# Optimization experiments

Hardware: AMD Instinct MI355X
Metric: run time of the kernel (lower is better)

## Reference

```python
import jax, jax.numpy as jnp
import numpy as np

D_MODEL = 1024
N_HEADS = 16
EPS = 1e-6


def setup_inputs() -> dict:
    key = jax.random.key(0)
    k1, k2, k3 = jax.random.split(key, 3)
    B, T, D = 2, 2048, D_MODEL
    x = jax.random.normal(k1, (B, T, D), dtype=jnp.float32)
    # learned params
    norm_weight = jnp.ones((D,), dtype=jnp.float32)
    qkv_w = jax.random.normal(k2, (3 * D, D), dtype=jnp.float32) * (1.0 / np.sqrt(D))
    out_w = jax.random.normal(k3, (D, D), dtype=jnp.float32) * (1.0 / np.sqrt(D))
    return {"x": x, "norm_weight": norm_weight, "qkv_w": qkv_w, "out_w": out_w}


def reference(x, norm_weight, qkv_w, out_w):
    B, T, D = x.shape
    H = N_HEADS
    d = D // H
    # RMSNorm
    ms = jnp.mean(x * x, axis=-1, keepdims=True)
    xn = x * jax.lax.rsqrt(ms + EPS) * norm_weight
    # QKV projection (Linear, no bias): y = x @ W^T
    qkv = jnp.einsum('btd,ed->bte', xn, qkv_w)  # (B,T,3D)
    q, k, v = jnp.split(qkv, 3, axis=-1)
    q = q.reshape(B, T, H, d)
    k = k.reshape(B, T, H, d)
    v = v.reshape(B, T, H, d)
    # scores (B,H,T,T) with causal mask
    scores = jnp.einsum('bqhd,bkhd->bhqk', q, k) / np.sqrt(d).astype(np.float32)
    causal = jnp.tril(jnp.ones((T, T), dtype=bool))
    scores = jnp.where(causal[None, None], scores, -jnp.inf)
    probs = jax.nn.softmax(scores, axis=-1)
    ctx = jnp.einsum('bhqk,bkhd->bqhd', probs, v)  # (B,T,H,d)
    out = ctx.reshape(B, T, D)
    out = jnp.einsum('btd,ed->bte', out, out_w)
    return out
```

## Files before the change

kernel.cpp:

```cpp
#include <hip/hip_runtime.h>
#include <stdint.h>

#define B_SZ 2
#define T_SZ 2048
#define DMODEL 1024
#define HCNT 16
#define HD 64
#define MROWS (B_SZ * T_SZ)

typedef __attribute__((ext_vector_type(8))) __bf16 bf16x8;
typedef __attribute__((ext_vector_type(4))) __bf16 bf16x4;
typedef __attribute__((ext_vector_type(4))) float f32x4;
typedef __attribute__((ext_vector_type(8))) unsigned short u16x8;

__device__ __forceinline__ unsigned short f2bf(float f) {
  union { float f; uint32_t u; } v; v.f = f;
  uint32_t u = v.u;
  u += 0x7fffu + ((u >> 16) & 1u);
  return (unsigned short)(u >> 16);
}

__device__ __forceinline__ float fexp2(float x) {
#if __has_builtin(__builtin_amdgcn_exp2f)
  return __builtin_amdgcn_exp2f(x);
#else
  return exp2f(x);
#endif
}

__device__ __forceinline__ void gld_lds16(const void* g, void* l) {
  __builtin_amdgcn_global_load_lds((__attribute__((address_space(1))) void*)(uintptr_t)g,
                                   (__attribute__((address_space(3))) void*)l, 16, 0, 0);
}

__global__ __launch_bounds__(256)
void cvt_all(const float* __restrict__ qkv_w, const float* __restrict__ out_w,
             unsigned short* __restrict__ dst) {
  int i = blockIdx.x * 256 + threadIdx.x;
  const int n1 = 3 * DMODEL * DMODEL / 4;
  float4 v = (i < n1) ? ((const float4*)qkv_w)[i] : ((const float4*)out_w)[i - n1];
  ushort4 o;
  o.x = f2bf(v.x); o.y = f2bf(v.y); o.z = f2bf(v.z); o.w = f2bf(v.w);
  ((ushort4*)dst)[i] = o;
}

__global__ __launch_bounds__(256)
void rmsnorm_bf16(const float* __restrict__ x, const float* __restrict__ w,
                  unsigned short* __restrict__ xn) {
  const int row = blockIdx.x;
  const int t = threadIdx.x;
  float4 v = ((const float4*)(x + (size_t)row * DMODEL))[t];
  float ss = v.x * v.x + v.y * v.y + v.z * v.z + v.w * v.w;
#pragma unroll
  for (int o = 1; o < 64; o <<= 1) ss += __shfl_xor(ss, o, 64);
  __shared__ float red[4];
  if ((t & 63) == 0) red[t >> 6] = ss;
  __syncthreads();
  float tot = red[0] + red[1] + red[2] + red[3];
  float scale = rsqrtf(tot * (1.0f / (float)DMODEL) + 1e-6f);
  float4 wv = ((const float4*)w)[t];
  ushort4 o;
  o.x = f2bf(v.x * scale * wv.x);
  o.y = f2bf(v.y * scale * wv.y);
  o.z = f2bf(v.z * scale * wv.z);
  o.w = f2bf(v.w * scale * wv.w);
  ((ushort4*)(xn + (size_t)row * DMODEL))[t] = o;
}

__device__ __forceinline__ void stage128x64(const unsigned short* g, int ldg,
                                            unsigned short* lds, int tid) {
  const int wave = tid >> 6;
#pragma unroll
  for (int i = 0; i < 4; ++i) {
    int row = i * 32 + (tid >> 3);
    const unsigned short* gp = g + (size_t)row * ldg + (((tid & 7) ^ (row & 7)) << 3);
    gld_lds16(gp, lds + i * 2048 + wave * 512);
  }
}

template <int F32OUT>
__global__ __launch_bounds__(256, 2)
void gemm_bt(const unsigned short* __restrict__ A, const unsigned short* __restrict__ B,
             void* __restrict__ Cv, int M, int N, int K, int nbx) {
  __shared__ __align__(16) unsigned short As[2][128 * 64];
  __shared__ __align__(16) unsigned short Bs[2][128 * 64];
  const int t = threadIdx.x, wave = t >> 6, lane = t & 63;
  const int cpx = gridDim.x >> 3;
  const int swz = (blockIdx.x & 7) * cpx + (blockIdx.x >> 3);
  const int m0 = (swz / nbx) * 128, n0 = (swz % nbx) * 128;
  const int wr = wave >> 1, wc = wave & 1;
  const int c = lane & 15, qg = lane >> 4;
  f32x4 acc[4][4] = {};
  const int nk = K >> 6;
  stage128x64(A + (size_t)m0 * K, K, As[0], t);
  stage128x64(B + (size_t)n0 * K, K, Bs[0], t);
  __syncthreads();
  int buf = 0;
  for (int kt = 0; kt < nk; ++kt) {
    if (kt + 1 < nk) {
      stage128x64(A + (size_t)m0 * K + (kt + 1) * 64, K, As[buf ^ 1], t);
      stage128x64(B + (size_t)n0 * K + (kt + 1) * 64, K, Bs[buf ^ 1], t);
    }
#pragma unroll
    for (int kk = 0; kk < 2; ++kk) {
      bf16x8 af[4], bfr[4];
#pragma unroll
      for (int mi = 0; mi < 4; ++mi) {
        int row = wr * 64 + mi * 16 + c;
        af[mi] = *(const bf16x8*)&As[buf][row * 64 + (((kk * 4 + qg) ^ (row & 7)) << 3)];
      }
#pragma unroll
      for (int ni = 0; ni < 4; ++ni) {
        int row = wc * 64 + ni * 16 + c;
        bfr[ni] = *(const bf16x8*)&Bs[buf][row * 64 + (((kk * 4 + qg) ^ (row & 7)) << 3)];
      }
#pragma unroll
      for (int mi = 0; mi < 4; ++mi)
#pragma unroll
        for (int ni = 0; ni < 4; ++ni)
          acc[mi][ni] = __builtin_amdgcn_mfma_f32_16x16x32_bf16(af[mi], bfr[ni], acc[mi][ni], 0, 0, 0);
    }
    __syncthreads();
    buf ^= 1;
  }
  const int cr = qg * 4;
#pragma unroll
  for (int mi = 0; mi < 4; ++mi)
#pragma unroll
    for (int ni = 0; ni < 4; ++ni) {
      int row = m0 + wr * 64 + mi * 16 + cr;
      int col = n0 + wc * 64 + ni * 16 + c;
      if (F32OUT) {
        float* C = (float*)Cv;
#pragma unroll
        for (int r = 0; r < 4; ++r) C[(size_t)(row + r) * N + col] = acc[mi][ni][r];
      } else {
        unsigned short* C = (unsigned short*)Cv;
#pragma unroll
        for (int r = 0; r < 4; ++r) C[(size_t)(row + r) * N + col] = f2bf(acc[mi][ni][r]);
      }
    }
}

__global__ __launch_bounds__(512, 2)
void attn_causal(const unsigned short* __restrict__ qkv, unsigned short* __restrict__ ctx) {
  __shared__ __align__(16) unsigned short Ks[2][128 * 64];
  __shared__ __align__(16) unsigned short Vt[2][2][64 * 72];
  __shared__ __align__(16) unsigned short Pl[8][32 * 136];
  const int tid = threadIdx.x, wave = tid >> 6, lane = tid & 63;
  const int id = blockIdx.x;
  const int bh = (id & 7) | ((id >> 6) << 3);
  const int p = (id >> 3) & 7;
  const int b = bh >> 4, h = bh & 15;
  const int q0a = p * 128 + wave * 16;
  const int q0b = (15 - p) * 128 + wave * 16;
  const int nit = 16 - p;
  const int c = lane & 15, qg = lane >> 4;
  const size_t base = (size_t)b * T_SZ * 3 * DMODEL;
  const int koffK = DMODEL + h * HD;
  const int koffV = 2 * DMODEL + h * HD;

  const float QSC = 0.125f * 1.4426950408889634f;
  bf16x8 aq[2][2];
#pragma unroll
  for (int mi = 0; mi < 2; ++mi)
#pragma unroll
    for (int kk = 0; kk < 2; ++kk) {
      int q = (mi ? q0b : q0a) + c;
      bf16x8 f = *(const bf16x8*)(qkv + base + (size_t)q * 3 * DMODEL + h * HD + kk * 32 + qg * 8);
#pragma unroll
      for (int j = 0; j < 8; ++j) f[j] = (__bf16)((float)f[j] * QSC);
      aq[mi][kk] = f;
    }

  float mst[2] = {-3e38f, -3e38f}, lst[2] = {0.f, 0.f};
  f32x4 aco[2][4];
#pragma unroll
  for (int mi = 0; mi < 2; ++mi)
#pragma unroll
    for (int nd = 0; nd < 4; ++nd)
#pragma unroll
      for (int r = 0; r < 4; ++r) aco[mi][nd][r] = 0.f;

  auto stageK = [&](int kb, int bufi) {
#pragma unroll
    for (int i = 0; i < 2; ++i) {
      int row = i * 64 + (tid >> 3);
      gld_lds16(qkv + base + (size_t)(kb + row) * 3 * DMODEL + koffK + (((tid & 7) ^ (row & 7)) << 3),
                &Ks[bufi][i * 4096 + (wave << 9)]);
    }
  };
  auto loadV = [&](int kb, u16x8* v) {
#pragma unroll
    for (int i = 0; i < 2; ++i)
      v[i] = *(const u16x8*)(qkv + base + (size_t)(kb + i * 64 + (tid >> 3)) * 3 * DMODEL + koffV + (tid & 7) * 8);
  };
  auto writeV = [&](int bufi, const u16x8* v) {
#pragma unroll
    for (int i = 0; i < 2; ++i) {
      int kv = tid >> 3;
#pragma unroll
      for (int j = 0; j < 8; ++j) {
        int dd = (tid & 7) * 8 + j;
        int f = (tid & 7) ^ j;
        Vt[bufi][i][dd * 72 + ((((kv >> 3) ^ f) << 3) | (kv & 7))] = v[i][j];
      }
    }
  };

  auto softmaxRow = [&](int mi, f32x4 s[8][2]) {
    float rm = -3e38f;
#pragma unroll
    for (int ni = 0; ni < 8; ++ni)
#pragma unroll
      for (int r = 0; r < 4; ++r) rm = fmaxf(rm, s[ni][mi][r]);
    rm = fmaxf(rm, __shfl_xor(rm, 16, 64));
    rm = fmaxf(rm, __shfl_xor(rm, 32, 64));
    float mo = mst[mi];
    float mn = mo;
    if (__any(rm > mo + 11.5f)) {
      mn = fmaxf(mo, rm);
      float corr = fexp2(mo - mn);
      lst[mi] *= corr;
      mst[mi] = mn;
#pragma unroll
      for (int r = 0; r < 4; ++r) {
        float cr = __shfl(corr, qg * 20 + r, 64);
#pragma unroll
        for (int nd = 0; nd < 4; ++nd) aco[mi][nd][r] *= cr;
      }
    }
    float rs = 0.f;
#pragma unroll
    for (int ni = 0; ni < 8; ++ni)
#pragma unroll
      for (int r = 0; r < 4; ++r) {
        float pv = fexp2(s[ni][mi][r] - mn);
        s[ni][mi][r] = pv;
        rs += pv;
      }
    rs += __shfl_xor(rs, 16, 64);
    rs += __shfl_xor(rs, 32, 64);
    lst[mi] += rs;
  };

  auto computeTile = [&](int kb, int kbuf, bool both, bool maskA, bool maskB) {
    f32x4 s[8][2] = {};
    __builtin_amdgcn_s_setprio(1);
#pragma unroll
    for (int kk = 0; kk < 2; ++kk) {
      bf16x8 bk[8];
#pragma unroll
      for (int ni = 0; ni < 8; ++ni) {
        int row = ni * 16 + c;
        int crd = kk * 4 + qg;
        bk[ni] = *(const bf16x8*)&Ks[kbuf][row * 64 + ((crd ^ (row & 7)) << 3)];
      }
#pragma unroll
      for (int ni = 0; ni < 8; ++ni)
        s[ni][1] = __builtin_amdgcn_mfma_f32_16x16x32_bf16(bk[ni], aq[1][kk], s[ni][1], 0, 0, 0);
      if (both)
#pragma unroll
        for (int ni = 0; ni < 8; ++ni)
          s[ni][0] = __builtin_amdgcn_mfma_f32_16x16x32_bf16(bk[ni], aq[0][kk], s[ni][0], 0, 0, 0);
    }
    __builtin_amdgcn_s_setprio(0);
    if (maskB) {
#pragma unroll
      for (int ni = 0; ni < 8; ++ni)
#pragma unroll
        for (int r = 0; r < 4; ++r) {
          int kg = kb + ni * 16 + qg * 4 + r;
          if (kg > q0b + c) s[ni][1][r] = -1e30f;
        }
    }
    if (both && maskA) {
#pragma unroll
      for (int ni = 0; ni < 8; ++ni)
#pragma unroll
        for (int r = 0; r < 4; ++r) {
          int kg = kb + ni * 16 + qg * 4 + r;
          if (kg > q0a + c) s[ni][0][r] = -1e30f;
        }
    }
    softmaxRow(1, s);
    if (both) softmaxRow(0, s);
    unsigned short* P = Pl[wave];
#pragma unroll
    for (int ni = 0; ni < 8; ++ni) {
      {
        bf16x4 pk;
#pragma unroll
        for (int r = 0; r < 4; ++r) pk[r] = (__bf16)s[ni][1][r];
        *(bf16x4*)&P[(16 + c) * 136 + ni * 16 + qg * 4] = pk;
      }
      if (both) {
        bf16x4 pk;
#pragma unroll
        for (int r = 0; r < 4; ++r) pk[r] = (__bf16)s[ni][0][r];
        *(bf16x4*)&P[c * 136 + ni * 16 + qg * 4] = pk;
      }
    }
    __builtin_amdgcn_s_setprio(1);
#pragma unroll
    for (int ch = 0; ch < 2; ++ch)
#pragma unroll
      for (int kk = 0; kk < 2; ++kk) {
        bf16x8 bv[4];
#pragma unroll
        for (int nd = 0; nd < 4; ++nd) {
          int dd = nd * 16 + c;
          int f = ((dd >> 3) ^ dd) & 7;
          int crd = kk * 4 + qg;
          bv[nd] = *(const bf16x8*)&Vt[kbuf][ch][dd * 72 + ((crd ^ f) << 3)];
        }
        bf16x8 pa1 = *(const bf16x8*)&P[(16 + c) * 136 + ch * 64 + kk * 32 + qg * 8];
#pragma unroll
        for (int nd = 0; nd < 4; ++nd)
          aco[1][nd] = __builtin_amdgcn_mfma_f32_16x16x32_bf16(pa1, bv[nd], aco[1][nd], 0, 0, 0);
        if (both) {
          bf16x8 pa0 = *(const bf16x8*)&P[c * 136 + ch * 64 + kk * 32 + qg * 8];
#pragma unroll
          for (int nd = 0; nd < 4; ++nd)
            aco[0][nd] = __builtin_amdgcn_mfma_f32_16x16x32_bf16(pa0, bv[nd], aco[0][nd], 0, 0, 0);
        }
      }
    __builtin_amdgcn_s_setprio(0);
  };

  stageK(0, 0);
  {
    u16x8 v0[2];
    loadV(0, v0);
    writeV(0, v0);
  }
  __syncthreads();
  int kbuf = 0;
  for (int t = 0; t < nit; ++t) {
    const int kb = t * 128;
    const bool hn = (t + 1 < nit);
    u16x8 vn[2];
    if (hn) { stageK(kb + 128, kbuf ^ 1); loadV(kb + 128, vn); }
    computeTile(kb, kbuf, t <= p, t == p, t == nit - 1);
    if (hn) writeV(kbuf ^ 1, vn);
    __syncthreads();
    kbuf ^= 1;
  }

  unsigned short* outp = ctx + (size_t)b * T_SZ * DMODEL + h * HD;
#pragma unroll
  for (int mi = 0; mi < 2; ++mi) {
    float linv = 1.f / lst[mi];
#pragma unroll
    for (int r = 0; r < 4; ++r) {
      float inv = __shfl(linv, qg * 20 + r, 64);
      int q = (mi ? q0b : q0a) + qg * 4 + r;
#pragma unroll
      for (int nd = 0; nd < 4; ++nd)
        outp[(size_t)q * DMODEL + nd * 16 + c] = f2bf(aco[mi][nd][r] * inv);
    }
  }
}

extern "C" void kernel_launch(void* const* d_in, const int* in_sizes, int n_in,
                              void* d_out, int out_size, void* d_ws, size_t ws_size,
                              hipStream_t stream) {
  const float* x = (const float*)d_in[0];
  const float* nw = (const float*)d_in[1];
  const float* qkv_w = (const float*)d_in[2];
  const float* out_w = (const float*)d_in[3];
  float* out = (float*)d_out;

  unsigned short* ws = (unsigned short*)d_ws;
  unsigned short* xn = ws;
  unsigned short* qkvw = xn + (size_t)MROWS * DMODEL;
  unsigned short* outw = qkvw + (size_t)3 * DMODEL * DMODEL;
  unsigned short* qkv = outw + (size_t)DMODEL * DMODEL;
  unsigned short* ctx = qkv + (size_t)MROWS * 3 * DMODEL;

  cvt_all<<<dim3(4096), dim3(256), 0, stream>>>(qkv_w, out_w, qkvw);
  rmsnorm_bf16<<<dim3(MROWS), dim3(256), 0, stream>>>(x, nw, xn);
  gemm_bt<0><<<dim3(768), dim3(256), 0, stream>>>(xn, qkvw, qkv, MROWS, 3 * DMODEL, DMODEL, 24);
  attn_causal<<<dim3(256), dim3(512), 0, stream>>>(qkv, ctx);
  gemm_bt<1><<<dim3(256), dim3(256), 0, stream>>>(ctx, outw, out, MROWS, DMODEL, DMODEL, 8);
}
```

Before: 122.6 us.

## Split attention blocks into 4-wave halves with 64-key tiles for more blocks

The causal attention kernel moves from 256 blocks of 8 waves to 512 blocks of 4 waves. Each block handles a 64-row half of a paired query strip and iterates over 64-key tiles instead of 128-key tiles, with shared buffers shrunk to match. Block-to-(b,h,p) mapping is also reordered to interleave light and heavy pairs. The aim is better CU fill and occupancy on the many-CU GPU, at the cost of more K/V tile loads and barriers per query row.

```diff
diff --git a/kernel.cpp b/kernel.cpp
--- a/kernel.cpp
+++ b/kernel.cpp
@@ -142,19 +142,22 @@
     }
 }
 
-__global__ __launch_bounds__(512, 2)
+__global__ __launch_bounds__(256, 3)
 void attn_causal(const unsigned short* __restrict__ qkv, unsigned short* __restrict__ ctx) {
-  __shared__ __align__(16) unsigned short Ks[2][128 * 64];
-  __shared__ __align__(16) unsigned short Vt[2][2][64 * 72];
-  __shared__ __align__(16) unsigned short Pl[8][32 * 136];
+  __shared__ __align__(16) unsigned short Ks[2][64 * 64];
+  __shared__ __align__(16) unsigned short Vt[2][64 * 72];
+  __shared__ __align__(16) unsigned short Pl[4][32 * 72];
   const int tid = threadIdx.x, wave = tid >> 6, lane = tid & 63;
   const int id = blockIdx.x;
-  const int bh = (id & 7) | ((id >> 6) << 3);
-  const int p = (id >> 3) & 7;
+  const int bh = (id & 7) | (((id >> 3) & 3) << 3);
+  const int k8 = (id >> 5) & 7;
+  const int half = (id >> 8) & 1;
+  int p = k8 >> 1; if (k8 & 1) p = 7 - p;
   const int b = bh >> 4, h = bh & 15;
-  const int q0a = p * 128 + wave * 16;
-  const int q0b = (15 - p) * 128 + wave * 16;
-  const int nit = 16 - p;
+  const int q0a = p * 128 + half * 64 + wave * 16;
+  const int q0b = (15 - p) * 128 + half * 64 + wave * 16;
+  const int tA = 2 * p + half;
+  const int nit = 2 * (15 - p) + half + 1;
   const int c = lane & 15, qg = lane >> 4;
   const size_t base = (size_t)b * T_SZ * 3 * DMODEL;
   const int koffK = DMODEL + h * HD;
@@ -185,33 +188,33 @@
   auto stageK = [&](int kb, int bufi) {
 #pragma unroll
     for (int i = 0; i < 2; ++i) {
-      int row = i * 64 + (tid >> 3);
+      int row = i * 32 + (tid >> 3);
       gld_lds16(qkv + base + (size_t)(kb + row) * 3 * DMODEL + koffK + (((tid & 7) ^ (row & 7)) << 3),
-                &Ks[bufi][i * 4096 + (wave << 9)]);
+                &Ks[bufi][i * 2048 + (wave << 9)]);
     }
   };
   auto loadV = [&](int kb, u16x8* v) {
 #pragma unroll
     for (int i = 0; i < 2; ++i)
-      v[i] = *(const u16x8*)(qkv + base + (size_t)(kb + i * 64 + (tid >> 3)) * 3 * DMODEL + koffV + (tid & 7) * 8);
+      v[i] = *(const u16x8*)(qkv + base + (size_t)(kb + i * 32 + (tid >> 3)) * 3 * DMODEL + koffV + (tid & 7) * 8);
   };
   auto writeV = [&](int bufi, const u16x8* v) {
 #pragma unroll
     for (int i = 0; i < 2; ++i) {
-      int kv = tid >> 3;
+      int kv = i * 32 + (tid >> 3);
 #pragma unroll
       for (int j = 0; j < 8; ++j) {
         int dd = (tid & 7) * 8 + j;
         int f = (tid & 7) ^ j;
-        Vt[bufi][i][dd * 72 + ((((kv >> 3) ^ f) << 3) | (kv & 7))] = v[i][j];
-      }
-    }
-  };
-
-  auto softmaxRow = [&](int mi, f32x4 s[8][2]) {
+        Vt[bufi][dd * 72 + ((((kv >> 3) ^ f) << 3) | (kv & 7))] = v[i][j];
+      }
+    }
+  };
+
+  auto softmaxRow = [&](int mi, f32x4 (&s)[4][2]) {
     float rm = -3e38f;
 #pragma unroll
-    for (int ni = 0; ni < 8; ++ni)
+    for (int ni = 0; ni < 4; ++ni)
 #pragma unroll
       for (int r = 0; r < 4; ++r) rm = fmaxf(rm, s[ni][mi][r]);
     rm = fmaxf(rm, __shfl_xor(rm, 16, 64));
@@ -232,7 +235,7 @@
     }
     float rs = 0.f;
 #pragma unroll
-    for (int ni = 0; ni < 8; ++ni)
+    for (int ni = 0; ni < 4; ++ni)
 #pragma unroll
       for (int r = 0; r < 4; ++r) {
         float pv = fexp2(s[ni][mi][r] - mn);
@@ -245,29 +248,29 @@
   };
 
   auto computeTile = [&](int kb, int kbuf, bool both, bool maskA, bool maskB) {
-    f32x4 s[8][2] = {};
+    f32x4 s[4][2] = {};
     __builtin_amdgcn_s_setprio(1);
 #pragma unroll
     for (int kk = 0; kk < 2; ++kk) {
-      bf16x8 bk[8];
-#pragma unroll
-      for (int ni = 0; ni < 8; ++ni) {
+      bf16x8 bk[4];
+#pragma unroll
+      for (int ni = 0; ni < 4; ++ni) {
         int row = ni * 16 + c;
         int crd = kk * 4 + qg;
         bk[ni] = *(const bf16x8*)&Ks[kbuf][row * 64 + ((crd ^ (row & 7)) << 3)];
       }
 #pragma unroll
-      for (int ni = 0; ni < 8; ++ni)
+      for (int ni = 0; ni < 4; ++ni)
         s[ni][1] = __builtin_amdgcn_mfma_f32_16x16x32_bf16(bk[ni], aq[1][kk], s[ni][1], 0, 0, 0);
       if (both)
 #pragma unroll
-        for (int ni = 0; ni < 8; ++ni)
+        for (int ni = 0; ni < 4; ++ni)
           s[ni][0] = __builtin_amdgcn_mfma_f32_16x16x32_bf16(bk[ni], aq[0][kk], s[ni][0], 0, 0, 0);
     }
     __builtin_amdgcn_s_setprio(0);
     if (maskB) {
 #pragma unroll
-      for (int ni = 0; ni < 8; ++ni)
+      for (int ni = 0; ni < 4; ++ni)
 #pragma unroll
         for (int r = 0; r < 4; ++r) {
           int kg = kb + ni * 16 + qg * 4 + r;
@@ -276,7 +279,7 @@
     }
     if (both && maskA) {
 #pragma unroll
-      for (int ni = 0; ni < 8; ++ni)
+      for (int ni = 0; ni < 4; ++ni)
 #pragma unroll
         for (int r = 0; r < 4; ++r) {
           int kg = kb + ni * 16 + qg * 4 + r;
@@ -287,44 +290,42 @@
     if (both) softmaxRow(0, s);
     unsigned short* P = Pl[wave];
 #pragma unroll
-    for (int ni = 0; ni < 8; ++ni) {
+    for (int ni = 0; ni < 4; ++ni) {
       {
         bf16x4 pk;
 #pragma unroll
         for (int r = 0; r < 4; ++r) pk[r] = (__bf16)s[ni][1][r];
-        *(bf16x4*)&P[(16 + c) * 136 + ni * 16 + qg * 4] = pk;
+        *(bf16x4*)&P[(16 + c) * 72 + ni * 16 + qg * 4] = pk;
       }
       if (both) {
         bf16x4 pk;
 #pragma unroll
         for (int r = 0; r < 4; ++r) pk[r] = (__bf16)s[ni][0][r];
-        *(bf16x4*)&P[c * 136 + ni * 16 + qg * 4] = pk;
+        *(bf16x4*)&P[c * 72 + ni * 16 + qg * 4] = pk;
       }
     }
     __builtin_amdgcn_s_setprio(1);
 #pragma unroll
-    for (int ch = 0; ch < 2; ++ch)
-#pragma unroll
-      for (int kk = 0; kk < 2; ++kk) {
-        bf16x8 bv[4];
-#pragma unroll
-        for (int nd = 0; nd < 4; ++nd) {
-          int dd = nd * 16 + c;
-          int f = ((dd >> 3) ^ dd) & 7;
-          int crd = kk * 4 + qg;
-          bv[nd] = *(const bf16x8*)&Vt[kbuf][ch][dd * 72 + ((crd ^ f) << 3)];
-        }
-        bf16x8 pa1 = *(const bf16x8*)&P[(16 + c) * 136 + ch * 64 + kk * 32 + qg * 8];
+    for (int kk = 0; kk < 2; ++kk) {
+      bf16x8 bv[4];
+#pragma unroll
+      for (int nd = 0; nd < 4; ++nd) {
+        int dd = nd * 16 + c;
+        int f = ((dd >> 3) ^ dd) & 7;
+        int crd = kk * 4 + qg;
+        bv[nd] = *(const bf16x8*)&Vt[kbuf][dd * 72 + ((crd ^ f) << 3)];
+      }
+      bf16x8 pa1 = *(const bf16x8*)&P[(16 + c) * 72 + kk * 32 + qg * 8];
+#pragma unroll
+      for (int nd = 0; nd < 4; ++nd)
+        aco[1][nd] = __builtin_amdgcn_mfma_f32_16x16x32_bf16(pa1, bv[nd], aco[1][nd], 0, 0, 0);
+      if (both) {
+        bf16x8 pa0 = *(const bf16x8*)&P[c * 72 + kk * 32 + qg * 8];
 #pragma unroll
         for (int nd = 0; nd < 4; ++nd)
-          aco[1][nd] = __builtin_amdgcn_mfma_f32_16x16x32_bf16(pa1, bv[nd], aco[1][nd], 0, 0, 0);
-        if (both) {
-          bf16x8 pa0 = *(const bf16x8*)&P[c * 136 + ch * 64 + kk * 32 + qg * 8];
-#pragma unroll
-          for (int nd = 0; nd < 4; ++nd)
-            aco[0][nd] = __builtin_amdgcn_mfma_f32_16x16x32_bf16(pa0, bv[nd], aco[0][nd], 0, 0, 0);
-        }
-      }
+          aco[0][nd] = __builtin_amdgcn_mfma_f32_16x16x32_bf16(pa0, bv[nd], aco[0][nd], 0, 0, 0);
+      }
+    }
     __builtin_amdgcn_s_setprio(0);
   };
 
@@ -337,11 +338,11 @@
   __syncthreads();
   int kbuf = 0;
   for (int t = 0; t < nit; ++t) {
-    const int kb = t * 128;
+    const int kb = t * 64;
     const bool hn = (t + 1 < nit);
     u16x8 vn[2];
-    if (hn) { stageK(kb + 128, kbuf ^ 1); loadV(kb + 128, vn); }
-    computeTile(kb, kbuf, t <= p, t == p, t == nit - 1);
+    if (hn) { stageK(kb + 64, kbuf ^ 1); loadV(kb + 64, vn); }
+    computeTile(kb, kbuf, t <= tA, t == tA, t == nit - 1);
     if (hn) writeV(kbuf ^ 1, vn);
     __syncthreads();
     kbuf ^= 1;
@@ -381,6 +382,6 @@
   cvt_all<<<dim3(4096), dim3(256), 0, stream>>>(qkv_w, out_w, qkvw);
   rmsnorm_bf16<<<dim3(MROWS), dim3(256), 0, stream>>>(x, nw, xn);
   gemm_bt<0><<<dim3(768), dim3(256), 0, stream>>>(xn, qkvw, qkv, MROWS, 3 * DMODEL, DMODEL, 24);
-  attn_causal<<<dim3(256), dim3(512), 0, stream>>>(qkv, ctx);
+  attn_causal<<<dim3(512), dim3(256), 0, stream>>>(qkv, ctx);
   gemm_bt<1><<<dim3(256), dim3(256), 0, stream>>>(ctx, outw, out, MROWS, DMODEL, DMODEL, 8);
 }
```

Measured after the change: 130.2 us. 6.2% more time.

## Split causal attention into 64-row query tiles with global K loads

Applied to the files above, without the earlier changes.

Replaces the paired-query-tile attention blocks (512 threads, two 128-row tiles per block) with smaller blocks of 256 threads that each handle one 64-row query tile. Blocks are ordered so the heaviest causal tiles launch first. K fragments are now read straight from global memory instead of being staged into LDS, and V uses a single LDS buffer guarded by two barriers. The aim is finer work distribution and lower LDS use per block for higher occupancy. The cost is redundant global/L2 reads of K across waves and the loss of K/V double buffering.

```diff
diff --git a/kernel.cpp b/kernel.cpp
--- a/kernel.cpp
+++ b/kernel.cpp
@@ -142,92 +142,101 @@
     }
 }
 
-__global__ __launch_bounds__(512, 2)
+__global__ __launch_bounds__(256, 4)
 void attn_causal(const unsigned short* __restrict__ qkv, unsigned short* __restrict__ ctx) {
-  __shared__ __align__(16) unsigned short Ks[2][128 * 64];
-  __shared__ __align__(16) unsigned short Vt[2][2][64 * 72];
-  __shared__ __align__(16) unsigned short Pl[8][32 * 136];
+  __shared__ __align__(16) unsigned short Vt[2][64 * 72];
+  __shared__ __align__(16) unsigned short Pl[4][16 * 136];
   const int tid = threadIdx.x, wave = tid >> 6, lane = tid & 63;
   const int id = blockIdx.x;
-  const int bh = (id & 7) | ((id >> 6) << 3);
-  const int p = (id >> 3) & 7;
+  const int bh = id & 31;
+  const int ts = id >> 5;
+  const int f = ts & 7, rank = ts >> 3;
+  const int qt = (rank == 0) ? (31 - f) : (rank == 1) ? f : (rank == 2) ? (16 + f) : (15 - f);
   const int b = bh >> 4, h = bh & 15;
-  const int q0a = p * 128 + wave * 16;
-  const int q0b = (15 - p) * 128 + wave * 16;
-  const int nit = 16 - p;
+  const int q0 = qt * 64 + wave * 16;
+  const int nit = (qt >> 1) + 1;
   const int c = lane & 15, qg = lane >> 4;
   const size_t base = (size_t)b * T_SZ * 3 * DMODEL;
-  const int koffK = DMODEL + h * HD;
-  const int koffV = 2 * DMODEL + h * HD;
+  const unsigned short* Kg = qkv + base + DMODEL + h * HD;
+  const unsigned short* Vg = qkv + base + 2 * DMODEL + h * HD;
 
   const float QSC = 0.125f * 1.4426950408889634f;
-  bf16x8 aq[2][2];
-#pragma unroll
-  for (int mi = 0; mi < 2; ++mi)
-#pragma unroll
-    for (int kk = 0; kk < 2; ++kk) {
-      int q = (mi ? q0b : q0a) + c;
-      bf16x8 f = *(const bf16x8*)(qkv + base + (size_t)q * 3 * DMODEL + h * HD + kk * 32 + qg * 8);
-#pragma unroll
-      for (int j = 0; j < 8; ++j) f[j] = (__bf16)((float)f[j] * QSC);
-      aq[mi][kk] = f;
-    }
-
-  float mst[2] = {-3e38f, -3e38f}, lst[2] = {0.f, 0.f};
-  f32x4 aco[2][4];
-#pragma unroll
-  for (int mi = 0; mi < 2; ++mi)
-#pragma unroll
-    for (int nd = 0; nd < 4; ++nd)
-#pragma unroll
-      for (int r = 0; r < 4; ++r) aco[mi][nd][r] = 0.f;
-
-  auto stageK = [&](int kb, int bufi) {
-#pragma unroll
-    for (int i = 0; i < 2; ++i) {
-      int row = i * 64 + (tid >> 3);
-      gld_lds16(qkv + base + (size_t)(kb + row) * 3 * DMODEL + koffK + (((tid & 7) ^ (row & 7)) << 3),
-                &Ks[bufi][i * 4096 + (wave << 9)]);
-    }
+  bf16x8 aq[2];
+#pragma unroll
+  for (int kk = 0; kk < 2; ++kk) {
+    bf16x8 q = *(const bf16x8*)(qkv + base + (size_t)(q0 + c) * 3 * DMODEL + h * HD + kk * 32 + qg * 8);
+#pragma unroll
+    for (int j = 0; j < 8; ++j) q[j] = (__bf16)((float)q[j] * QSC);
+    aq[kk] = q;
+  }
+
+  float mst = -3e38f, lst = 0.f;
+  f32x4 aco[4];
+#pragma unroll
+  for (int nd = 0; nd < 4; ++nd)
+#pragma unroll
+    for (int r = 0; r < 4; ++r) aco[nd][r] = 0.f;
+
+  auto loadV = [&](int kb, u16x8* v) {
+#pragma unroll
+    for (int i = 0; i < 4; ++i)
+      v[i] = *(const u16x8*)(Vg + (size_t)(kb + i * 32 + (tid >> 3)) * 3 * DMODEL + (tid & 7) * 8);
   };
-  auto loadV = [&](int kb, u16x8* v) {
-#pragma unroll
-    for (int i = 0; i < 2; ++i)
-      v[i] = *(const u16x8*)(qkv + base + (size_t)(kb + i * 64 + (tid >> 3)) * 3 * DMODEL + koffV + (tid & 7) * 8);
-  };
-  auto writeV = [&](int bufi, const u16x8* v) {
-#pragma unroll
-    for (int i = 0; i < 2; ++i) {
-      int kv = tid >> 3;
+  auto writeV = [&](const u16x8* v) {
+#pragma unroll
+    for (int i = 0; i < 4; ++i) {
+      int ch = i >> 1;
+      int kv = (i & 1) * 32 + (tid >> 3);
 #pragma unroll
       for (int j = 0; j < 8; ++j) {
         int dd = (tid & 7) * 8 + j;
-        int f = (tid & 7) ^ j;
-        Vt[bufi][i][dd * 72 + ((((kv >> 3) ^ f) << 3) | (kv & 7))] = v[i][j];
+        int ff = (tid & 7) ^ j;
+        Vt[ch][dd * 72 + ((((kv >> 3) ^ ff) << 3) | (kv & 7))] = v[i][j];
       }
     }
   };
 
-  auto softmaxRow = [&](int mi, f32x4 s[8][2]) {
+  auto computeTile = [&](int kb, bool domask) {
+    f32x4 s[8] = {};
+    __builtin_amdgcn_s_setprio(1);
+#pragma unroll
+    for (int kk = 0; kk < 2; ++kk) {
+      bf16x8 bk[8];
+#pragma unroll
+      for (int ni = 0; ni < 8; ++ni)
+        bk[ni] = *(const bf16x8*)(Kg + (size_t)(kb + ni * 16 + c) * 3 * DMODEL + kk * 32 + qg * 8);
+#pragma unroll
+      for (int ni = 0; ni < 8; ++ni)
+        s[ni] = __builtin_amdgcn_mfma_f32_16x16x32_bf16(bk[ni], aq[kk], s[ni], 0, 0, 0);
+    }
+    __builtin_amdgcn_s_setprio(0);
+    if (domask) {
+#pragma unroll
+      for (int ni = 0; ni < 8; ++ni)
+#pragma unroll
+        for (int r = 0; r < 4; ++r) {
+          int kg = kb + ni * 16 + qg * 4 + r;
+          if (kg > q0 + c) s[ni][r] = -1e30f;
+        }
+    }
     float rm = -3e38f;
 #pragma unroll
     for (int ni = 0; ni < 8; ++ni)
 #pragma unroll
-      for (int r = 0; r < 4; ++r) rm = fmaxf(rm, s[ni][mi][r]);
+      for (int r = 0; r < 4; ++r) rm = fmaxf(rm, s[ni][r]);
     rm = fmaxf(rm, __shfl_xor(rm, 16, 64));
     rm = fmaxf(rm, __shfl_xor(rm, 32, 64));
-    float mo = mst[mi];
-    float mn = mo;
+    float mo = mst, mn = mo;
     if (__any(rm > mo + 11.5f)) {
       mn = fmaxf(mo, rm);
       float corr = fexp2(mo - mn);
-      lst[mi] *= corr;
-      mst[mi] = mn;
+      lst *= corr;
+      mst = mn;
 #pragma unroll
       for (int r = 0; r < 4; ++r) {
         float cr = __shfl(corr, qg * 20 + r, 64);
 #pragma unroll
-        for (int nd = 0; nd < 4; ++nd) aco[mi][nd][r] *= cr;
+        for (int nd = 0; nd < 4; ++nd) aco[nd][r] *= cr;
       }
     }
     float rs = 0.f;
@@ -235,71 +244,20 @@
     for (int ni = 0; ni < 8; ++ni)
 #pragma unroll
       for (int r = 0; r < 4; ++r) {
-        float pv = fexp2(s[ni][mi][r] - mn);
-        s[ni][mi][r] = pv;
+        float pv = fexp2(s[ni][r] - mn);
+        s[ni][r] = pv;
         rs += pv;
       }
     rs += __shfl_xor(rs, 16, 64);
     rs += __shfl_xor(rs, 32, 64);
-    lst[mi] += rs;
-  };
-
-  auto computeTile = [&](int kb, int kbuf, bool both, bool maskA, bool maskB) {
-    f32x4 s[8][2] = {};
-    __builtin_amdgcn_s_setprio(1);
-#pragma unroll
-    for (int kk = 0; kk < 2; ++kk) {
-      bf16x8 bk[8];
-#pragma unroll
-      for (int ni = 0; ni < 8; ++ni) {
-        int row = ni * 16 + c;
-        int crd = kk * 4 + qg;
-        bk[ni] = *(const bf16x8*)&Ks[kbuf][row * 64 + ((crd ^ (row & 7)) << 3)];
-      }
-#pragma unroll
-      for (int ni = 0; ni < 8; ++ni)
-        s[ni][1] = __builtin_amdgcn_mfma_f32_16x16x32_bf16(bk[ni], aq[1][kk], s[ni][1], 0, 0, 0);
-      if (both)
-#pragma unroll
-        for (int ni = 0; ni < 8; ++ni)
-          s[ni][0] = __builtin_amdgcn_mfma_f32_16x16x32_bf16(bk[ni], aq[0][kk], s[ni][0], 0, 0, 0);
-    }
-    __builtin_amdgcn_s_setprio(0);
-    if (maskB) {
-#pragma unroll
-      for (int ni = 0; ni < 8; ++ni)
-#pragma unroll
-        for (int r = 0; r < 4; ++r) {
-          int kg = kb + ni * 16 + qg * 4 + r;
-          if (kg > q0b + c) s[ni][1][r] = -1e30f;
-        }
-    }
-    if (both && maskA) {
-#pragma unroll
-      for (int ni = 0; ni < 8; ++ni)
-#pragma unroll
-        for (int r = 0; r < 4; ++r) {
-          int kg = kb + ni * 16 + qg * 4 + r;
-          if (kg > q0a + c) s[ni][0][r] = -1e30f;
-        }
-    }
-    softmaxRow(1, s);
-    if (both) softmaxRow(0, s);
+    lst += rs;
     unsigned short* P = Pl[wave];
 #pragma unroll
     for (int ni = 0; ni < 8; ++ni) {
-      {
-        bf16x4 pk;
-#pragma unroll
-        for (int r = 0; r < 4; ++r) pk[r] = (__bf16)s[ni][1][r];
-        *(bf16x4*)&P[(16 + c) * 136 + ni * 16 + qg * 4] = pk;
-      }
-      if (both) {
-        bf16x4 pk;
-#pragma unroll
-        for (int r = 0; r < 4; ++r) pk[r] = (__bf16)s[ni][0][r];
-        *(bf16x4*)&P[c * 136 + ni * 16 + qg * 4] = pk;
-      }
+      bf16x4 pk;
+#pragma unroll
+      for (int r = 0; r < 4; ++r) pk[r] = (__bf16)s[ni][r];
+      *(bf16x4*)&P[c * 136 + ni * 16 + qg * 4] = pk;
     }
     __builtin_amdgcn_s_setprio(1);
 #pragma unroll
@@ -310,55 +268,43 @@
 #pragma unroll
         for (int nd = 0; nd < 4; ++nd) {
           int dd = nd * 16 + c;
-          int f = ((dd >> 3) ^ dd) & 7;
+          int ff = ((dd >> 3) ^ dd) & 7;
           int crd = kk * 4 + qg;
-          bv[nd] = *(const bf16x8*)&Vt[kbuf][ch][dd * 72 + ((crd ^ f) << 3)];
+          bv[nd] = *(const bf16x8*)&Vt[ch][dd * 72 + ((crd ^ ff) << 3)];
         }
-        bf16x8 pa1 = *(const bf16x8*)&P[(16 + c) * 136 + ch * 64 + kk * 32 + qg * 8];
+        bf16x8 pa = *(const bf16x8*)&P[c * 136 + ch * 64 + kk * 32 + qg * 8];
 #pragma unroll
         for (int nd = 0; nd < 4; ++nd)
-          aco[1][nd] = __builtin_amdgcn_mfma_f32_16x16x32_bf16(pa1, bv[nd], aco[1][nd], 0, 0, 0);
-        if (both) {
-          bf16x8 pa0 = *(const bf16x8*)&P[c * 136 + ch * 64 + kk * 32 + qg * 8];
-#pragma unroll
-          for (int nd = 0; nd < 4; ++nd)
-            aco[0][nd] = __builtin_amdgcn_mfma_f32_16x16x32_bf16(pa0, bv[nd], aco[0][nd], 0, 0, 0);
-        }
+          aco[nd] = __builtin_amdgcn_mfma_f32_16x16x32_bf16(pa, bv[nd], aco[nd], 0, 0, 0);
       }
     __builtin_amdgcn_s_setprio(0);
   };
 
-  stageK(0, 0);
-  {
-    u16x8 v0[2];
-    loadV(0, v0);
-    writeV(0, v0);
-  }
+  u16x8 vn[4];
+  loadV(0, vn);
+  writeV(vn);
   __syncthreads();
-  int kbuf = 0;
   for (int t = 0; t < nit; ++t) {
     const int kb = t * 128;
     const bool hn = (t + 1 < nit);
-    u16x8 vn[2];
-    if (hn) { stageK(kb + 128, kbuf ^ 1); loadV(kb + 128, vn); }
-    computeTile(kb, kbuf, t <= p, t == p, t == nit - 1);
-    if (hn) writeV(kbuf ^ 1, vn);
-    __syncthreads();
-    kbuf ^= 1;
+    if (hn) loadV(kb + 128, vn);
+    computeTile(kb, t == nit - 1);
+    if (hn) {
+      __syncthreads();
+      writeV(vn);
+      __syncthreads();
+    }
   }
 
   unsigned short* outp = ctx + (size_t)b * T_SZ * DMODEL + h * HD;
-#pragma unroll
-  for (int mi = 0; mi < 2; ++mi) {
-    float linv = 1.f / lst[mi];
-#pragma unroll
-    for (int r = 0; r < 4; ++r) {
-      float inv = __shfl(linv, qg * 20 + r, 64);
-      int q = (mi ? q0b : q0a) + qg * 4 + r;
-#pragma unroll
-      for (int nd = 0; nd < 4; ++nd)
-        outp[(size_t)q * DMODEL + nd * 16 + c] = f2bf(aco[mi][nd][r] * inv);
-    }
+  float linv = 1.f / lst;
+#pragma unroll
+  for (int r = 0; r < 4; ++r) {
+    float inv = __shfl(linv, qg * 20 + r, 64);
+    int q = q0 + qg * 4 + r;
+#pragma unroll
+    for (int nd = 0; nd < 4; ++nd)
+      outp[(size_t)q * DMODEL + nd * 16 + c] = f2bf(aco[nd][r] * inv);
   }
 }
 
@@ -381,6 +327,6 @@
   cvt_all<<<dim3(4096), dim3(256), 0, stream>>>(qkv_w, out_w, qkvw);
   rmsnorm_bf16<<<dim3(MROWS), dim3(256), 0, stream>>>(x, nw, xn);
   gemm_bt<0><<<dim3(768), dim3(256), 0, stream>>>(xn, qkvw, qkv, MROWS, 3 * DMODEL, DMODEL, 24);
-  attn_causal<<<dim3(256), dim3(512), 0, stream>>>(qkv, ctx);
+  attn_causal<<<dim3(1024), dim3(256), 0, stream>>>(qkv, ctx);
   gemm_bt<1><<<dim3(256), dim3(256), 0, stream>>>(ctx, outw, out, MROWS, DMODEL, DMODEL, 8);
 }
```

Measured after the change: 165.2 us. +34.7%, slower.

## Split attention blocks into 4-wave halves and shrink per-wave P staging buffer

Applied to the files above, without the earlier changes.

The attention kernel moves from 256 blocks of 8 waves to 512 blocks of 4 waves. Each block covers half of a paired query tile, and blocks are reordered so the two halves take mirrored causal pair indices, which balances work. The P (probability) staging buffer is cut from a full 128-column row per wave to a 32-column slice that is written just before each MFMA chunk, reducing LDS use so more blocks fit per CU. In exchange, each K/V tile is now loaded by twice as many blocks, which raises global/L2 traffic, and the extra P writes and reads within the loop add LDS round trips.

```diff
diff --git a/kernel.cpp b/kernel.cpp
--- a/kernel.cpp
+++ b/kernel.cpp
@@ -142,23 +142,25 @@
     }
 }
 
-__global__ __launch_bounds__(512, 2)
+__global__ __launch_bounds__(256, 2)
 void attn_causal(const unsigned short* __restrict__ qkv, unsigned short* __restrict__ ctx) {
   __shared__ __align__(16) unsigned short Ks[2][128 * 64];
   __shared__ __align__(16) unsigned short Vt[2][2][64 * 72];
-  __shared__ __align__(16) unsigned short Pl[8][32 * 136];
+  __shared__ __align__(16) unsigned short Pl[4][32 * 40];
   const int tid = threadIdx.x, wave = tid >> 6, lane = tid & 63;
   const int id = blockIdx.x;
-  const int bh = (id & 7) | ((id >> 6) << 3);
-  const int p = (id >> 3) & 7;
+  const int bh = id & 31;
+  const int ph = (id >> 5) & 7;
+  const int half = (id >> 8) & 1;
+  const int p = half ? 7 - ph : ph;
   const int b = bh >> 4, h = bh & 15;
-  const int q0a = p * 128 + wave * 16;
-  const int q0b = (15 - p) * 128 + wave * 16;
+  const int q0a = p * 128 + half * 64 + wave * 16;
+  const int q0b = (15 - p) * 128 + half * 64 + wave * 16;
   const int nit = 16 - p;
   const int c = lane & 15, qg = lane >> 4;
   const size_t base = (size_t)b * T_SZ * 3 * DMODEL;
-  const int koffK = DMODEL + h * HD;
-  const int koffV = 2 * DMODEL + h * HD;
+  const unsigned short* Kg = qkv + base + DMODEL + h * HD;
+  const unsigned short* Vg = qkv + base + 2 * DMODEL + h * HD;
 
   const float QSC = 0.125f * 1.4426950408889634f;
   bf16x8 aq[2][2];
@@ -167,10 +169,10 @@
 #pragma unroll
     for (int kk = 0; kk < 2; ++kk) {
       int q = (mi ? q0b : q0a) + c;
-      bf16x8 f = *(const bf16x8*)(qkv + base + (size_t)q * 3 * DMODEL + h * HD + kk * 32 + qg * 8);
-#pragma unroll
-      for (int j = 0; j < 8; ++j) f[j] = (__bf16)((float)f[j] * QSC);
-      aq[mi][kk] = f;
+      bf16x8 fq = *(const bf16x8*)(qkv + base + (size_t)q * 3 * DMODEL + h * HD + kk * 32 + qg * 8);
+#pragma unroll
+      for (int j = 0; j < 8; ++j) fq[j] = (__bf16)((float)fq[j] * QSC);
+      aq[mi][kk] = fq;
     }
 
   float mst[2] = {-3e38f, -3e38f}, lst[2] = {0.f, 0.f};
@@ -184,31 +186,32 @@
 
   auto stageK = [&](int kb, int bufi) {
 #pragma unroll
-    for (int i = 0; i < 2; ++i) {
-      int row = i * 64 + (tid >> 3);
-      gld_lds16(qkv + base + (size_t)(kb + row) * 3 * DMODEL + koffK + (((tid & 7) ^ (row & 7)) << 3),
-                &Ks[bufi][i * 4096 + (wave << 9)]);
+    for (int i = 0; i < 4; ++i) {
+      int row = i * 32 + (tid >> 3);
+      gld_lds16(Kg + (size_t)(kb + row) * 3 * DMODEL + (((tid & 7) ^ (row & 7)) << 3),
+                &Ks[bufi][i * 2048 + (wave << 9)]);
     }
   };
   auto loadV = [&](int kb, u16x8* v) {
 #pragma unroll
-    for (int i = 0; i < 2; ++i)
-      v[i] = *(const u16x8*)(qkv + base + (size_t)(kb + i * 64 + (tid >> 3)) * 3 * DMODEL + koffV + (tid & 7) * 8);
+    for (int i = 0; i < 4; ++i)
+      v[i] = *(const u16x8*)(Vg + (size_t)(kb + i * 32 + (tid >> 3)) * 3 * DMODEL + (tid & 7) * 8);
   };
   auto writeV = [&](int bufi, const u16x8* v) {
 #pragma unroll
-    for (int i = 0; i < 2; ++i) {
-      int kv = tid >> 3;
+    for (int i = 0; i < 4; ++i) {
+      int ch = i >> 1;
+      int kv = (i & 1) * 32 + (tid >> 3);
 #pragma unroll
       for (int j = 0; j < 8; ++j) {
         int dd = (tid & 7) * 8 + j;
-        int f = (tid & 7) ^ j;
-        Vt[bufi][i][dd * 72 + ((((kv >> 3) ^ f) << 3) | (kv & 7))] = v[i][j];
-      }
-    }
-  };
-
-  auto softmaxRow = [&](int mi, f32x4 s[8][2]) {
+        int ff = (tid & 7) ^ j;
+        Vt[bufi][ch][dd * 72 + ((((kv >> 3) ^ ff) << 3) | (kv & 7))] = v[i][j];
+      }
+    }
+  };
+
+  auto softmaxRow = [&](int mi, f32x4 (&s)[8][2]) {
     float rm = -3e38f;
 #pragma unroll
     for (int ni = 0; ni < 8; ++ni)
@@ -286,43 +289,42 @@
     softmaxRow(1, s);
     if (both) softmaxRow(0, s);
     unsigned short* P = Pl[wave];
-#pragma unroll
-    for (int ni = 0; ni < 8; ++ni) {
-      {
-        bf16x4 pk;
-#pragma unroll
-        for (int r = 0; r < 4; ++r) pk[r] = (__bf16)s[ni][1][r];
-        *(bf16x4*)&P[(16 + c) * 136 + ni * 16 + qg * 4] = pk;
-      }
-      if (both) {
-        bf16x4 pk;
-#pragma unroll
-        for (int r = 0; r < 4; ++r) pk[r] = (__bf16)s[ni][0][r];
-        *(bf16x4*)&P[c * 136 + ni * 16 + qg * 4] = pk;
-      }
-    }
     __builtin_amdgcn_s_setprio(1);
 #pragma unroll
     for (int ch = 0; ch < 2; ++ch)
 #pragma unroll
       for (int kk = 0; kk < 2; ++kk) {
+#pragma unroll
+        for (int par = 0; par < 2; ++par) {
+          int ni = ch * 4 + kk * 2 + par;
+          bf16x4 pkB;
+#pragma unroll
+          for (int r = 0; r < 4; ++r) pkB[r] = (__bf16)s[ni][1][r];
+          *(bf16x4*)&P[(16 + c) * 40 + par * 16 + qg * 4] = pkB;
+          if (both) {
+            bf16x4 pkA;
+#pragma unroll
+            for (int r = 0; r < 4; ++r) pkA[r] = (__bf16)s[ni][0][r];
+            *(bf16x4*)&P[c * 40 + par * 16 + qg * 4] = pkA;
+          }
+        }
         bf16x8 bv[4];
 #pragma unroll
         for (int nd = 0; nd < 4; ++nd) {
           int dd = nd * 16 + c;
-          int f = ((dd >> 3) ^ dd) & 7;
+          int ff = ((dd >> 3) ^ dd) & 7;
           int crd = kk * 4 + qg;
-          bv[nd] = *(const bf16x8*)&Vt[kbuf][ch][dd * 72 + ((crd ^ f) << 3)];
-        }
-        bf16x8 pa1 = *(const bf16x8*)&P[(16 + c) * 136 + ch * 64 + kk * 32 + qg * 8];
+          bv[nd] = *(const bf16x8*)&Vt[kbuf][ch][dd * 72 + ((crd ^ ff) << 3)];
+        }
+        bf16x8 paB = *(const bf16x8*)&P[(16 + c) * 40 + qg * 8];
 #pragma unroll
         for (int nd = 0; nd < 4; ++nd)
-          aco[1][nd] = __builtin_amdgcn_mfma_f32_16x16x32_bf16(pa1, bv[nd], aco[1][nd], 0, 0, 0);
+          aco[1][nd] = __builtin_amdgcn_mfma_f32_16x16x32_bf16(paB, bv[nd], aco[1][nd], 0, 0, 0);
         if (both) {
-          bf16x8 pa0 = *(const bf16x8*)&P[c * 136 + ch * 64 + kk * 32 + qg * 8];
+          bf16x8 paA = *(const bf16x8*)&P[c * 40 + qg * 8];
 #pragma unroll
           for (int nd = 0; nd < 4; ++nd)
-            aco[0][nd] = __builtin_amdgcn_mfma_f32_16x16x32_bf16(pa0, bv[nd], aco[0][nd], 0, 0, 0);
+            aco[0][nd] = __builtin_amdgcn_mfma_f32_16x16x32_bf16(paA, bv[nd], aco[0][nd], 0, 0, 0);
         }
       }
     __builtin_amdgcn_s_setprio(0);
@@ -330,7 +332,7 @@
 
   stageK(0, 0);
   {
-    u16x8 v0[2];
+    u16x8 v0[4];
     loadV(0, v0);
     writeV(0, v0);
   }
@@ -339,7 +341,7 @@
   for (int t = 0; t < nit; ++t) {
     const int kb = t * 128;
     const bool hn = (t + 1 < nit);
-    u16x8 vn[2];
+    u16x8 vn[4];
     if (hn) { stageK(kb + 128, kbuf ^ 1); loadV(kb + 128, vn); }
     computeTile(kb, kbuf, t <= p, t == p, t == nit - 1);
     if (hn) writeV(kbuf ^ 1, vn);
@@ -381,6 +383,6 @@
   cvt_all<<<dim3(4096), dim3(256), 0, stream>>>(qkv_w, out_w, qkvw);
   rmsnorm_bf16<<<dim3(MROWS), dim3(256), 0, stream>>>(x, nw, xn);
   gemm_bt<0><<<dim3(768), dim3(256), 0, stream>>>(xn, qkvw, qkv, MROWS, 3 * DMODEL, DMODEL, 24);
-  attn_causal<<<dim3(256), dim3(512), 0, stream>>>(qkv, ctx);
+  attn_causal<<<dim3(512), dim3(256), 0, stream>>>(qkv, ctx);
   gemm_bt<1><<<dim3(256), dim3(256), 0, stream>>>(ctx, outw, out, MROWS, DMODEL, DMODEL, 8);
 }
```

Result: no change. 122.1 us (-0.4%).
